# Performance work log

Measured on AMD Instinct MI355X. Metric: run time of the kernel, lower is better.

## Reference

```python
import jax, jax.numpy as jnp
import numpy as np

VOCAB = 50257
D_MODEL = 1024
PAD_IDX = 0
B, L = 4, 4096


def setup_inputs() -> dict:
    key = jax.random.key(0)
    k1, k2, k3, k4, k5 = jax.random.split(key, 5)
    input_ids = jax.random.randint(k1, (B, L), 0, VOCAB, dtype=jnp.int64 if jax.config.jax_enable_x64 else jnp.int32)
    role_mask = jax.random.randint(k2, (B, L), 0, 2, dtype=input_ids.dtype)
    emb = jax.random.normal(k3, (VOCAB, D_MODEL), dtype=jnp.float32)
    emb = emb.at[PAD_IDX].set(0.0)  # padding_idx row is zero in nn.Embedding
    # nn.Linear weight has shape (out, in); y = x @ W.T
    scale = 1.0 / np.sqrt(D_MODEL)
    W0 = jax.random.uniform(k4, (D_MODEL, D_MODEL), dtype=jnp.float32, minval=-scale, maxval=scale)
    W1 = jax.random.uniform(k5, (D_MODEL, D_MODEL), dtype=jnp.float32, minval=-scale, maxval=scale)
    return {"input_ids": input_ids, "role_mask": role_mask, "emb": emb, "W0": W0, "W1": W1}


def reference(input_ids, role_mask, emb, W0, W1):
    # Embedding lookup: (B, L, D)
    x = emb[input_ids]
    # Per-role linear transform (2-expert routing); compute both, select by mask.
    y0 = jnp.einsum('bld,ed->ble', x, W0)
    y1 = jnp.einsum('bld,ed->ble', x, W1)
    out = jnp.where((role_mask == 1)[..., None], y1, y0)
    return out
```

## Files before the change

### kernel.cpp

```cpp
#include <hip/hip_runtime.h>


#define M_TOK   16384
#define DIM     1024
#define MT      128
#define NTIL    130
#define XROWS   (NTIL * MT)
#define BK      64
#define PBLK    64
#define WBLKS   2048
#define GROWS   8

typedef __attribute__((ext_vector_type(8))) short short8;
typedef __attribute__((ext_vector_type(4))) float f32x4;

#define OFF_PERM 256
#define OFF_WB   66816
#define OFF_X    4261120

static __device__ __forceinline__ unsigned short f2bf(float f) {
    unsigned int u = __float_as_uint(f);
    u += 0x7fffu + ((u >> 16) & 1u);
    return (unsigned short)(u >> 16);
}

__global__ void k_pre(const int* __restrict__ role, int* perm, int* cnt,
                      const float* __restrict__ W0, const float* __restrict__ W1,
                      unsigned short* __restrict__ Wb) {
    int b = blockIdx.x;
    if (b < PBLK) {
        int t = b * 256 + threadIdx.x;
        int row;
        if (role[t] == 1) { int s = atomicAdd(&cnt[1], 1); row = XROWS - 1 - s; }
        else              { int s = atomicAdd(&cnt[0], 1); row = s; }
        perm[row] = t;
    } else {
        int idx = ((b - PBLK) * 256 + threadIdx.x) * 4;
        const float* src = (idx < 1048576) ? (W0 + idx) : (W1 + (idx - 1048576));
        float4 f = *(const float4*)src;
        *(ushort4*)(Wb + idx) = make_ushort4(f2bf(f.x), f2bf(f.y), f2bf(f.z), f2bf(f.w));
    }
}

__global__ void k_gather(const int* __restrict__ ids, const int* __restrict__ perm,
                         const int* __restrict__ cnt, const float* __restrict__ emb,
                         unsigned short* __restrict__ X) {
    int base = blockIdx.x * GROWS;
    int n0 = cnt[0], n1 = cnt[1];
    int t = threadIdx.x;
#pragma unroll
    for (int r = 0; r < GROWS; ++r) {
        int row = base + r;
        if (row >= n0 && row < XROWS - n1) continue;
        int p  = perm[row];
        int id = ids[p];
        float4 f = *(const float4*)(emb + (size_t)id * DIM + t * 4);
        *(ushort4*)(X + (size_t)row * DIM + t * 4) =
            make_ushort4(f2bf(f.x), f2bf(f.y), f2bf(f.z), f2bf(f.w));
    }
}

__global__ __launch_bounds__(256, 3)
void k_gemm(const unsigned short* __restrict__ Xu, const unsigned short* __restrict__ Wbu,
            const int* __restrict__ perm, const int* __restrict__ cnt,
            float* __restrict__ out) {
    __shared__ short As[MT * BK];
    __shared__ short Bs[MT * BK];

    int f  = blockIdx.x;
    int mt = ((f >> 6) << 3) | (f & 7);
    int nt = (f >> 3) & 7;
    if (mt >= NTIL) return;

    int n0 = cnt[0], n1 = cnt[1];
    int T0 = (n0 + 127) >> 7, T1 = (n1 + 127) >> 7;
    int e, lo, hi;
    if (mt < T0)              { e = 0; lo = 0;            hi = n0;    }
    else if (mt >= NTIL - T1) { e = 1; lo = XROWS - n1;   hi = XROWS; }
    else return;

    const short* Ag = (const short*)Xu + (size_t)mt * MT * DIM;
    const short* Bg = (const short*)Wbu + (size_t)e * DIM * DIM + (size_t)nt * MT * DIM;

    int tid  = threadIdx.x;
    int lane = tid & 63;
    int w    = tid >> 6;
    int wm   = w & 1, wn = w >> 1;
    int quad = lane >> 4, lq = lane & 15;

    f32x4 acc[4][4] = {};

    for (int k0 = 0; k0 < DIM; k0 += BK) {
#pragma unroll
        for (int i = 0; i < 4; ++i) {
            int q   = w * 4 + i;
            int s   = q * 64 + lane;
            int row = s >> 3;
            int kc  = (s & 7) ^ (row & 7);
            __builtin_amdgcn_global_load_lds(
                (const __attribute__((address_space(1))) unsigned int*)(Ag + (size_t)row * DIM + k0 + kc * 8),
                (__attribute__((address_space(3))) unsigned int*)(&As[s * 8]),
                16, 0, 0);
            __builtin_amdgcn_global_load_lds(
                (const __attribute__((address_space(1))) unsigned int*)(Bg + (size_t)row * DIM + k0 + kc * 8),
                (__attribute__((address_space(3))) unsigned int*)(&Bs[s * 8]),
                16, 0, 0);
        }
        __syncthreads();

#pragma unroll
        for (int s = 0; s < 2; ++s) {
            short8 av[4], bv[4];
            int s4q = s * 4 + quad;
#pragma unroll
            for (int i = 0; i < 4; ++i) {
                int ra = wm * 64 + i * 16 + lq;
                av[i] = *(const short8*)&As[(ra * 8 + (s4q ^ (ra & 7))) * 8];
                int rb = wn * 64 + i * 16 + lq;
                bv[i] = *(const short8*)&Bs[(rb * 8 + (s4q ^ (rb & 7))) * 8];
            }
#pragma unroll
            for (int i = 0; i < 4; ++i)
#pragma unroll
                for (int j = 0; j < 4; ++j)
                    acc[i][j] = __builtin_amdgcn_mfma_f32_16x16x32_bf16(
                        av[i], bv[j], acc[i][j], 0, 0, 0);
        }
        __syncthreads();
    }

    int colbase = nt * 128 + wn * 64 + lq;
#pragma unroll
    for (int i = 0; i < 4; ++i) {
#pragma unroll
        for (int r = 0; r < 4; ++r) {
            int mrow = mt * MT + wm * 64 + i * 16 + quad * 4 + r;
            if (mrow < lo || mrow >= hi) continue;
            int token = perm[mrow];
            float* o = out + (size_t)token * DIM + colbase;
#pragma unroll
            for (int j = 0; j < 4; ++j)
                o[j * 16] = acc[i][j][r];
        }
    }
}

extern "C" void kernel_launch(void* const* d_in, const int* in_sizes, int n_in,
                              void* d_out, int out_size, void* d_ws, size_t ws_size,
                              hipStream_t stream) {
    const int*   ids  = (const int*)d_in[0];
    const int*   role = (const int*)d_in[1];
    const float* emb  = (const float*)d_in[2];
    const float* W0   = (const float*)d_in[3];
    const float* W1   = (const float*)d_in[4];
    float*       out  = (float*)d_out;

    char* ws = (char*)d_ws;
    int* cnt  = (int*)ws;
    int* perm = (int*)(ws + OFF_PERM);
    unsigned short* Wb = (unsigned short*)(ws + OFF_WB);
    unsigned short* X  = (unsigned short*)(ws + OFF_X);

    hipMemsetAsync(cnt, 0x00, 2 * sizeof(int), stream);
    k_pre   <<<PBLK + WBLKS,  256, 0, stream>>>(role, perm, cnt, W0, W1, Wb);
    k_gather<<<XROWS / GROWS, 256, 0, stream>>>(ids, perm, cnt, emb, X);
    k_gemm  <<<1088,          256, 0, stream>>>(X, Wb, perm, cnt, out);
}
```

Baseline: 332.0 us.

## Fuse embedding gather into pre-kernel and gather rows via perm in GEMM

The separate gather kernel is removed. Embedding rows are now converted to bf16 in token order inside the pre-kernel, running in parallel with the role partitioning and weight conversion. The GEMM instead looks up each A-tile row's token through perm and precomputes those row offsets once per block. This saves one kernel launch and the serial dependency on the partition, at the cost of non-contiguous A-row loads in the GEMM.

```diff
diff --git a/kernel.cpp b/kernel.cpp
--- a/kernel.cpp
+++ b/kernel.cpp
@@ -10,6 +10,7 @@
 #define PBLK    64
 #define WBLKS   2048
 #define GROWS   8
+#define GBLK    (M_TOK / GROWS)
 
 typedef __attribute__((ext_vector_type(8))) short short8;
 typedef __attribute__((ext_vector_type(4))) float f32x4;
@@ -24,9 +25,11 @@
     return (unsigned short)(u >> 16);
 }
 
-__global__ void k_pre(const int* __restrict__ role, int* perm, int* cnt,
+__global__ void k_pre(const int* __restrict__ role, const int* __restrict__ ids,
+                      int* perm, int* cnt,
                       const float* __restrict__ W0, const float* __restrict__ W1,
-                      unsigned short* __restrict__ Wb) {
+                      unsigned short* __restrict__ Wb,
+                      const float* __restrict__ emb, unsigned short* __restrict__ X) {
     int b = blockIdx.x;
     if (b < PBLK) {
         int t = b * 256 + threadIdx.x;
@@ -34,29 +37,22 @@
         if (role[t] == 1) { int s = atomicAdd(&cnt[1], 1); row = XROWS - 1 - s; }
         else              { int s = atomicAdd(&cnt[0], 1); row = s; }
         perm[row] = t;
-    } else {
+    } else if (b < PBLK + WBLKS) {
         int idx = ((b - PBLK) * 256 + threadIdx.x) * 4;
         const float* src = (idx < 1048576) ? (W0 + idx) : (W1 + (idx - 1048576));
         float4 f = *(const float4*)src;
         *(ushort4*)(Wb + idx) = make_ushort4(f2bf(f.x), f2bf(f.y), f2bf(f.z), f2bf(f.w));
-    }
-}
-
-__global__ void k_gather(const int* __restrict__ ids, const int* __restrict__ perm,
-                         const int* __restrict__ cnt, const float* __restrict__ emb,
-                         unsigned short* __restrict__ X) {
-    int base = blockIdx.x * GROWS;
-    int n0 = cnt[0], n1 = cnt[1];
-    int t = threadIdx.x;
+    } else {
+        int t0  = (b - PBLK - WBLKS) * GROWS;
+        int tid = threadIdx.x;
 #pragma unroll
-    for (int r = 0; r < GROWS; ++r) {
-        int row = base + r;
-        if (row >= n0 && row < XROWS - n1) continue;
-        int p  = perm[row];
-        int id = ids[p];
-        float4 f = *(const float4*)(emb + (size_t)id * DIM + t * 4);
-        *(ushort4*)(X + (size_t)row * DIM + t * 4) =
-            make_ushort4(f2bf(f.x), f2bf(f.y), f2bf(f.z), f2bf(f.w));
+        for (int r = 0; r < GROWS; ++r) {
+            int tok = t0 + r;
+            int id  = ids[tok];
+            float4 f = *(const float4*)(emb + (size_t)id * DIM + tid * 4);
+            *(ushort4*)(X + (size_t)tok * DIM + tid * 4) =
+                make_ushort4(f2bf(f.x), f2bf(f.y), f2bf(f.z), f2bf(f.w));
+        }
     }
 }
 
@@ -79,7 +75,7 @@
     else if (mt >= NTIL - T1) { e = 1; lo = XROWS - n1;   hi = XROWS; }
     else return;
 
-    const short* Ag = (const short*)Xu + (size_t)mt * MT * DIM;
+    const short* Xg = (const short*)Xu;
     const short* Bg = (const short*)Wbu + (size_t)e * DIM * DIM + (size_t)nt * MT * DIM;
 
     int tid  = threadIdx.x;
@@ -88,22 +84,32 @@
     int wm   = w & 1, wn = w >> 1;
     int quad = lane >> 4, lq = lane & 15;
 
+    unsigned int aoff[4], boff[4];
+    int sA[4];
+#pragma unroll
+    for (int i = 0; i < 4; ++i) {
+        int s    = (w * 4 + i) * 64 + lane;
+        int row  = s >> 3;
+        int kc   = (s & 7) ^ (row & 7);
+        int grow = mt * MT + row;
+        int prow = (grow >= lo && grow < hi) ? perm[grow] : 0;
+        sA[i]   = s;
+        aoff[i] = (unsigned int)prow * DIM + (unsigned int)kc * 8;
+        boff[i] = (unsigned int)(row * DIM + kc * 8);
+    }
+
     f32x4 acc[4][4] = {};
 
     for (int k0 = 0; k0 < DIM; k0 += BK) {
 #pragma unroll
         for (int i = 0; i < 4; ++i) {
-            int q   = w * 4 + i;
-            int s   = q * 64 + lane;
-            int row = s >> 3;
-            int kc  = (s & 7) ^ (row & 7);
             __builtin_amdgcn_global_load_lds(
-                (const __attribute__((address_space(1))) unsigned int*)(Ag + (size_t)row * DIM + k0 + kc * 8),
-                (__attribute__((address_space(3))) unsigned int*)(&As[s * 8]),
+                (const __attribute__((address_space(1))) unsigned int*)(Xg + aoff[i] + k0),
+                (__attribute__((address_space(3))) unsigned int*)(&As[sA[i] * 8]),
                 16, 0, 0);
             __builtin_amdgcn_global_load_lds(
-                (const __attribute__((address_space(1))) unsigned int*)(Bg + (size_t)row * DIM + k0 + kc * 8),
-                (__attribute__((address_space(3))) unsigned int*)(&Bs[s * 8]),
+                (const __attribute__((address_space(1))) unsigned int*)(Bg + boff[i] + k0),
+                (__attribute__((address_space(3))) unsigned int*)(&Bs[sA[i] * 8]),
                 16, 0, 0);
         }
         __syncthreads();
@@ -162,7 +168,6 @@
     unsigned short* X  = (unsigned short*)(ws + OFF_X);
 
     hipMemsetAsync(cnt, 0x00, 2 * sizeof(int), stream);
-    k_pre   <<<PBLK + WBLKS,  256, 0, stream>>>(role, perm, cnt, W0, W1, Wb);
-    k_gather<<<XROWS / GROWS, 256, 0, stream>>>(ids, perm, cnt, emb, X);
-    k_gemm  <<<1088,          256, 0, stream>>>(X, Wb, perm, cnt, out);
+    k_pre <<<PBLK + WBLKS + GBLK, 256, 0, stream>>>(role, ids, perm, cnt, W0, W1, Wb, emb, X);
+    k_gemm<<<1088,                256, 0, stream>>>(X, Wb, perm, cnt, out);
 }
```

After: 322.3 us. 2.9% less time.
